# Kernel tuning notes

Hardware: AMD Instinct MI355X
Metric: run time of the kernel (lower is better)

The kernel has to match this reference:

```python
import jax, jax.numpy as jnp
import numpy as np

N_NODES = 100000
N_EDGES = 1600000
N_GRAPHS = 256
F_IN = 38
HID = 64


def graph_conv(x, edge_index, w_rel, b_rel, w_root):
    # PyG GraphConv (aggr='add'): out = lin_rel(sum_{j in N(i)} x_j) + lin_root(x_i)
    src, dst = edge_index[0], edge_index[1]
    agg = jax.ops.segment_sum(x[src], dst, num_segments=N_NODES)  # [N, F]
    return agg @ w_rel + b_rel + x @ w_root


def setup_inputs() -> dict:
    key = jax.random.key(0)
    ks = jax.random.split(key, 10)
    x = jax.random.normal(ks[0], (N_NODES, F_IN), dtype=jnp.float32)
    edge_index = jax.random.randint(ks[1], (2, N_EDGES), 0, N_NODES, dtype=jnp.int64)
    batch = jnp.sort(jax.random.randint(ks[2], (N_NODES,), 0, N_GRAPHS, dtype=jnp.int64))
    s1 = 1.0 / np.sqrt(F_IN)
    s2 = 1.0 / np.sqrt(HID)
    w1_rel = jax.random.uniform(ks[3], (F_IN, HID), jnp.float32, -s1, s1)
    b1_rel = jax.random.uniform(ks[4], (HID,), jnp.float32, -s1, s1)
    w1_root = jax.random.uniform(ks[5], (F_IN, HID), jnp.float32, -s1, s1)
    w2_rel = jax.random.uniform(ks[6], (HID, HID), jnp.float32, -s2, s2)
    b2_rel = jax.random.uniform(ks[7], (HID,), jnp.float32, -s2, s2)
    w2_root = jax.random.uniform(ks[8], (HID, HID), jnp.float32, -s2, s2)
    return {"x": x, "edge_index": edge_index, "batch": batch,
            "w1_rel": w1_rel, "b1_rel": b1_rel, "w1_root": w1_root,
            "w2_rel": w2_rel, "b2_rel": b2_rel, "w2_root": w2_root}


def reference(x, edge_index, batch, w1_rel, b1_rel, w1_root, w2_rel, b2_rel, w2_root):
    h = graph_conv(x, edge_index, w1_rel, b1_rel, w1_root)
    h = jax.nn.relu(h)
    h = graph_conv(h, edge_index, w2_rel, b2_rel, w2_root)
    # global_mean_pool: segment mean over batch ids
    sums = jax.ops.segment_sum(h, batch, num_segments=N_GRAPHS)  # [G, HID]
    counts = jax.ops.segment_sum(jnp.ones((N_NODES,), h.dtype), batch, num_segments=N_GRAPHS)
    pooled = sums / jnp.maximum(counts, 1.0)[:, None]
    # dropout(p=0.5, training=False) is identity in eval mode
    return jax.nn.relu(pooled)
```

## Files before the change

### kernel.cpp

```cpp
#include <hip/hip_runtime.h>

#define N_NODES 100000
#define N_EDGES 1600000
#define N_GRAPHS 256
#define F_IN 38
#define F_PAD 40
#define HID 64
#define CAPD 48

#define NB   391
#define EPB  4096
#define EDGE_BLOCKS 391
#define PACK_BLOCKS 1024
#define PACK_CHUNKS ((N_NODES + 1) * F_PAD / 8)
#define BCAP 4608
#define NBL  (2 * NB)

typedef unsigned short ushort;
typedef unsigned int uint;
typedef _Float16 h2 __attribute__((ext_vector_type(2)));

__device__ __forceinline__ h2 u2h(uint u) {
    union { uint u; h2 h; } v; v.u = u; return v.h;
}
__device__ __forceinline__ uint h2u(h2 h) {
    union { uint u; h2 h; } v; v.h = h; return v.u;
}
__device__ __forceinline__ ushort f2h_bits(float f) {
    union { _Float16 h; ushort s; } v; v.h = (_Float16)f; return v.s;
}
__device__ __forceinline__ int clampi(int v) {
    return (int)min((uint)v, (uint)N_NODES);
}

__global__ __launch_bounds__(256, 4) void pre_kernel(
        const float* __restrict__ x,
        const int* __restrict__ src,
        const int* __restrict__ dst,
        int* __restrict__ gcur,
        uint* __restrict__ ebuf,
        ushort* __restrict__ xb,
        ushort* __restrict__ hb) {
    __shared__ int    hist[NB];
    __shared__ int    offs[NB];
    __shared__ int    cur[NB];
    __shared__ int    gbase[NB];
    __shared__ int    scan[512];
    __shared__ uint   sbuf[EPB];
    __shared__ ushort sb[EPB];

    const int blk = blockIdx.x;
    if (blk >= EDGE_BLOCKS) {
        int gid = (blk - EDGE_BLOCKS) * 256 + threadIdx.x;
        if (gid < HID) hb[(N_NODES << 6) + gid] = 0;
        const int stride = PACK_BLOCKS * 256;
        for (int c = gid; c < PACK_CHUNKS; c += stride) {
            int n = c / 5;
            int f0 = (c - n * 5) * 8;
            ushort u[8];
            #pragma unroll
            for (int j = 0; j < 8; ++j) {
                int f = f0 + j;
                float v = (n < N_NODES && f < F_IN) ? x[n * F_IN + f] : 0.0f;
                u[j] = f2h_bits(v);
            }
            uint4 pk;
            pk.x = (uint)u[0] | ((uint)u[1] << 16);
            pk.y = (uint)u[2] | ((uint)u[3] << 16);
            pk.z = (uint)u[4] | ((uint)u[5] << 16);
            pk.w = (uint)u[6] | ((uint)u[7] << 16);
            *(uint4*)(xb + c * 8) = pk;
        }
        return;
    }

    for (int i = threadIdx.x; i < NB; i += 256) hist[i] = 0;
    __syncthreads();

    const int base = blk * EPB + threadIdx.x;
    int  bkt[EPB / 256];
    uint pl[EPB / 256];
    #pragma unroll
    for (int i = 0; i < EPB / 256; ++i) {
        int e = base + i * 256;
        bkt[i] = -1;
        if (e < N_EDGES) {
            int d = dst[e];
            bkt[i] = d >> 8;
            pl[i] = ((uint)src[e] << 8) | ((uint)d & 255u);
            atomicAdd(&hist[bkt[i]], 1);
        }
    }
    __syncthreads();

    {
        int i0 = threadIdx.x, i1 = threadIdx.x + 256;
        scan[i0] = (i0 < NB) ? hist[i0] : 0;
        scan[i1] = (i1 < NB) ? hist[i1] : 0;
        __syncthreads();
        for (int d = 1; d < 512; d <<= 1) {
            int v0 = (i0 >= d) ? scan[i0 - d] : 0;
            int v1 = (i1 >= d) ? scan[i1 - d] : 0;
            __syncthreads();
            scan[i0] += v0;
            scan[i1] += v1;
            __syncthreads();
        }
    }
    for (int i = threadIdx.x; i < NB; i += 256) {
        int h = hist[i];
        int o = scan[i] - h;
        offs[i] = o;
        cur[i] = o;
        gbase[i] = (h > 0) ? atomicAdd(&gcur[i], h) : 0;
    }
    __syncthreads();

    #pragma unroll
    for (int i = 0; i < EPB / 256; ++i) {
        if (bkt[i] >= 0) {
            int pos = atomicAdd(&cur[bkt[i]], 1);
            sbuf[pos] = pl[i];
            sb[pos] = (ushort)bkt[i];
        }
    }
    __syncthreads();

    int total = scan[NB - 1];
    for (int i = threadIdx.x; i < total; i += 256) {
        int b = sb[i];
        int p = gbase[b] + (i - offs[b]);
        if (p < BCAP) ebuf[b * BCAP + p] = sbuf[i];
    }
}

__global__ __launch_bounds__(512, 8) void layer1_kernel(
        const uint* __restrict__ xb32,
        const uint* __restrict__ ebuf,
        const int* __restrict__ gcur,
        const float* __restrict__ w_rel,
        const float* __restrict__ b_rel,
        const float* __restrict__ w_root,
        const int* __restrict__ batch,
        ushort* __restrict__ hb,
        float* __restrict__ hsum) {
    __shared__ uint s_wrelp[20 * HID];
    __shared__ uint s_wrootp[20 * HID];
    __shared__ int  s_slots[128 * CAPD];
    __shared__ int  cl[128];

    for (int i = threadIdx.x; i < 20 * HID; i += 512) {
        int kk = i >> 6, cc = i & 63;
        int k0 = 2 * kk, k1 = 2 * kk + 1;
        float r0 = (k0 < F_IN) ? w_rel[k0 * HID + cc] : 0.f;
        float r1 = (k1 < F_IN) ? w_rel[k1 * HID + cc] : 0.f;
        float o0 = (k0 < F_IN) ? w_root[k0 * HID + cc] : 0.f;
        float o1 = (k1 < F_IN) ? w_root[k1 * HID + cc] : 0.f;
        s_wrelp[i]  = (uint)f2h_bits(r0) | ((uint)f2h_bits(r1) << 16);
        s_wrootp[i] = (uint)f2h_bits(o0) | ((uint)f2h_bits(o1) << 16);
    }
    const int b   = blockIdx.x >> 1;
    const int dlo = (blockIdx.x & 1) << 7;
    if (threadIdx.x < 128) cl[threadIdx.x] = 0;
    {
        int4* sp = (int4*)s_slots;
        int4 dummy = make_int4(N_NODES, N_NODES, N_NODES, N_NODES);
        for (int i = threadIdx.x; i < 128 * CAPD / 4; i += 512) sp[i] = dummy;
    }
    __syncthreads();
    int e1 = gcur[b]; if (e1 > BCAP) e1 = BCAP;
    for (int idx = threadIdx.x; idx < e1; idx += 512) {
        uint e = ebuf[b * BCAP + idx];
        int dl = (int)(e & 255u) - dlo;
        if ((uint)dl < 128u) {
            int pos = atomicAdd(&cl[dl], 1);
            if (pos < CAPD) s_slots[dl * CAPD + pos] = (int)(e >> 8);
        }
    }
    __syncthreads();

    const int wave = threadIdx.x >> 6, lane = threadIdx.x & 63;
    const int half = lane >> 5, l32 = lane & 31;
    const int nbase = (b << 8) + dlo;

    h2   sums[8];
    uint xvs[8];
    #pragma unroll
    for (int i = 0; i < 8; ++i) {
        int nl = wave * 16 + 2 * i + half;
        int n = nbase + nl;
        uint xv = 0;
        int dp = 0;
        if (n < N_NODES) {
            int deg = cl[nl]; if (deg > CAPD) deg = CAPD;
            dp = (deg + 15) & ~15; if (dp > CAPD) dp = CAPD;
            if (l32 < 20) xv = xb32[n * 20 + l32];
        }
        h2 sum = {(_Float16)0, (_Float16)0};
        const int* sl = s_slots + nl * CAPD;
        for (int j = 0; j < dp; j += 16) {
            int4 a4 = *(const int4*)(sl + j);
            int4 b4 = *(const int4*)(sl + j + 4);
            int4 c4 = *(const int4*)(sl + j + 8);
            int4 d4 = *(const int4*)(sl + j + 12);
            if (l32 < 20) {
                uint v0 = xb32[clampi(a4.x) * 20 + l32];
                uint v1 = xb32[clampi(a4.y) * 20 + l32];
                uint v2 = xb32[clampi(a4.z) * 20 + l32];
                uint v3 = xb32[clampi(a4.w) * 20 + l32];
                uint v4 = xb32[clampi(b4.x) * 20 + l32];
                uint v5 = xb32[clampi(b4.y) * 20 + l32];
                uint v6 = xb32[clampi(b4.z) * 20 + l32];
                uint v7 = xb32[clampi(b4.w) * 20 + l32];
                uint v8 = xb32[clampi(c4.x) * 20 + l32];
                uint v9 = xb32[clampi(c4.y) * 20 + l32];
                uint va = xb32[clampi(c4.z) * 20 + l32];
                uint vb = xb32[clampi(c4.w) * 20 + l32];
                uint vc = xb32[clampi(d4.x) * 20 + l32];
                uint vd = xb32[clampi(d4.y) * 20 + l32];
                uint ve = xb32[clampi(d4.z) * 20 + l32];
                uint vf = xb32[clampi(d4.w) * 20 + l32];
                h2 t0 = (u2h(v0) + u2h(v1)) + (u2h(v2) + u2h(v3));
                h2 t1 = (u2h(v4) + u2h(v5)) + (u2h(v6) + u2h(v7));
                h2 t2 = (u2h(v8) + u2h(v9)) + (u2h(va) + u2h(vb));
                h2 t3 = (u2h(vc) + u2h(vd)) + (u2h(ve) + u2h(vf));
                sum += (t0 + t1) + (t2 + t3);
            }
        }
        sums[i] = sum;
        xvs[i] = xv;
    }
    __syncthreads();
    uint* s_a = (uint*)s_slots;
    uint* s_x = ((uint*)s_slots) + 128 * 20;
    #pragma unroll
    for (int i = 0; i < 8; ++i) {
        int nl = wave * 16 + 2 * i + half;
        if (l32 < 20) {
            s_a[nl * 20 + l32] = h2u(sums[i]);
            s_x[nl * 20 + l32] = xvs[i];
        }
    }
    __syncthreads();

    const int c = lane, r = wave;
    const float bias = b_rel[c];
    float psum = 0.f;
    int cur_g = -1;
    for (int i = 0; i < 16; ++i) {
        int nl = r * 16 + i;
        int n = nbase + nl;
        if (n >= N_NODES) break;
        h2 acc = {(_Float16)0, (_Float16)0};
        #pragma unroll
        for (int k8 = 0; k8 < 5; ++k8) {
            uint4 pa = *(const uint4*)&s_a[nl * 20 + k8 * 4];
            uint4 px = *(const uint4*)&s_x[nl * 20 + k8 * 4];
            acc += u2h(pa.x) * u2h(s_wrelp[(k8 * 4 + 0) * HID + c]);
            acc += u2h(pa.y) * u2h(s_wrelp[(k8 * 4 + 1) * HID + c]);
            acc += u2h(pa.z) * u2h(s_wrelp[(k8 * 4 + 2) * HID + c]);
            acc += u2h(pa.w) * u2h(s_wrelp[(k8 * 4 + 3) * HID + c]);
            acc += u2h(px.x) * u2h(s_wrootp[(k8 * 4 + 0) * HID + c]);
            acc += u2h(px.y) * u2h(s_wrootp[(k8 * 4 + 1) * HID + c]);
            acc += u2h(px.z) * u2h(s_wrootp[(k8 * 4 + 2) * HID + c]);
            acc += u2h(px.w) * u2h(s_wrootp[(k8 * 4 + 3) * HID + c]);
        }
        float hv = fmaxf((float)acc.x + (float)acc.y + bias, 0.f);
        hb[(n << 6) + c] = f2h_bits(hv);
        int g = batch[n];
        if (g != cur_g) {
            if (cur_g >= 0) atomicAdd(&hsum[(cur_g << 6) + c], psum);
            psum = 0.f;
            cur_g = g;
        }
        psum += hv;
    }
    if (cur_g >= 0) atomicAdd(&hsum[(cur_g << 6) + c], psum);
}

__global__ __launch_bounds__(256, 8) void layer2_kernel(
        const uint* __restrict__ hb32,
        const uint* __restrict__ ebuf,
        const int* __restrict__ gcur,
        const int* __restrict__ batch,
        float* __restrict__ esum) {
    __shared__ int   s_batch[256];
    __shared__ float s_acc[4 * 64];

    const int b = blockIdx.x >> 2;
    const int q = blockIdx.x & 3;
    const int nbase = b << 8;
    {
        int n = nbase + threadIdx.x;
        s_batch[threadIdx.x] = (n < N_NODES) ? batch[n] : (N_GRAPHS - 1);
    }
    s_acc[threadIdx.x] = 0.f;
    __syncthreads();
    const int g0 = s_batch[0];

    int e1 = gcur[b]; if (e1 > BCAP) e1 = BCAP;
    const int lo = (e1 * q) >> 2;
    const int hi = (e1 * (q + 1)) >> 2;

    const int wave = threadIdx.x >> 6, lane = threadIdx.x & 63;
    const int hf = lane >> 5, l32 = lane & 31;
    const uint* eb = ebuf + b * BCAP;

    float a0x = 0.f, a0y = 0.f, a1x = 0.f, a1y = 0.f;
    float a2x = 0.f, a2y = 0.f, a3x = 0.f, a3y = 0.f;

    for (int base = lo + (wave << 6); base < hi; base += 256) {
        int cnt = hi - base; if (cnt > 64) cnt = 64;
        uint pv = (lane < cnt) ? eb[base + lane] : 0u;
        #pragma unroll 8
        for (int k = 0; k < 32; ++k) {
            int idx2 = 2 * k + hf;
            uint p = __shfl(pv, idx2, 64);
            if (idx2 < cnt) {
                int srcn = (int)(p >> 8);
                int g = s_batch[p & 255u];
                int off = g - g0;
                h2 hv = u2h(hb32[(srcn << 5) + l32]);
                float hx = (float)hv.x, hy = (float)hv.y;
                if (off == 0)      { a0x += hx; a0y += hy; }
                else if (off == 1) { a1x += hx; a1y += hy; }
                else if (off == 2) { a2x += hx; a2y += hy; }
                else if (off == 3) { a3x += hx; a3y += hy; }
                else {
                    atomicAdd(&esum[(g << 6) + 2 * l32], hx);
                    atomicAdd(&esum[(g << 6) + 2 * l32 + 1], hy);
                }
            }
        }
    }
    atomicAdd(&s_acc[0 * 64 + 2 * l32],     a0x);
    atomicAdd(&s_acc[0 * 64 + 2 * l32 + 1], a0y);
    atomicAdd(&s_acc[1 * 64 + 2 * l32],     a1x);
    atomicAdd(&s_acc[1 * 64 + 2 * l32 + 1], a1y);
    atomicAdd(&s_acc[2 * 64 + 2 * l32],     a2x);
    atomicAdd(&s_acc[2 * 64 + 2 * l32 + 1], a2y);
    atomicAdd(&s_acc[3 * 64 + 2 * l32],     a3x);
    atomicAdd(&s_acc[3 * 64 + 2 * l32 + 1], a3y);
    __syncthreads();
    {
        int off = threadIdx.x >> 6, ch = threadIdx.x & 63;
        int g = g0 + off;
        float v = s_acc[off * 64 + ch];
        if (v != 0.f && g < N_GRAPHS)
            atomicAdd(&esum[(g << 6) + ch], v);
    }
}

__global__ void finalize_kernel(const float* __restrict__ esum,
                                const float* __restrict__ hsum,
                                const float* __restrict__ w2_rel,
                                const float* __restrict__ w2_root,
                                const float* __restrict__ b2,
                                const int* __restrict__ batch,
                                float* __restrict__ out) {
    __shared__ float s_e[HID];
    __shared__ float s_h[HID];
    const int g = blockIdx.x;
    const int c = threadIdx.x;
    s_e[c] = esum[(g << 6) + c];
    s_h[c] = hsum[(g << 6) + c];
    __syncthreads();

    int lo = 0, hi = N_NODES;
    while (lo < hi) { int m = (lo + hi) >> 1; if (batch[m] < g) lo = m + 1; else hi = m; }
    int start = lo;
    hi = N_NODES;
    while (lo < hi) { int m = (lo + hi) >> 1; if (batch[m] < g + 1) lo = m + 1; else hi = m; }
    int cntg = lo - start;

    float acc = (float)cntg * b2[c];
    #pragma unroll
    for (int k = 0; k < HID; ++k) {
        acc += s_e[k] * w2_rel[k * HID + c];
        acc += s_h[k] * w2_root[k * HID + c];
    }
    float denom = cntg > 0 ? (float)cntg : 1.f;
    out[(g << 6) + c] = fmaxf(acc / denom, 0.f);
}

extern "C" void kernel_launch(void* const* d_in, const int* in_sizes, int n_in,
                              void* d_out, int out_size, void* d_ws, size_t ws_size,
                              hipStream_t stream) {
    const float* x       = (const float*)d_in[0];
    const int*   ei      = (const int*)  d_in[1];
    const int*   batch   = (const int*)  d_in[2];
    const float* w1_rel  = (const float*)d_in[3];
    const float* b1_rel  = (const float*)d_in[4];
    const float* w1_root = (const float*)d_in[5];
    const float* w2_rel  = (const float*)d_in[6];
    const float* b2_rel  = (const float*)d_in[7];
    const float* w2_root = (const float*)d_in[8];
    float* out = (float*)d_out;

    const int* src = ei;
    const int* dst = ei + N_EDGES;

    char* wsb = (char*)d_ws;
    float*  hsum  = (float*) (wsb);
    float*  esum  = (float*) (wsb + 65536);
    int*    gcur  = (int*)   (wsb + 131072);
    uint*   ebuf  = (uint*)  (wsb + 132672);
    ushort* xb    = (ushort*)(wsb + 19732640);
    ushort* hb    = (ushort*)(wsb + 27732720);

    hipMemsetAsync(wsb, 0, 132636, stream);

    {
        pre_kernel<<<EDGE_BLOCKS + PACK_BLOCKS, 256, 0, stream>>>(
            x, src, dst, gcur, ebuf, xb, hb);
    }
    {
        layer1_kernel<<<NBL, 512, 0, stream>>>((const uint*)xb, ebuf, gcur,
                                               w1_rel, b1_rel, w1_root, batch,
                                               hb, hsum);
    }
    {
        layer2_kernel<<<4 * NB, 256, 0, stream>>>((const uint*)hb, ebuf, gcur,
                                                  batch, esum);
    }
    {
        finalize_kernel<<<N_GRAPHS, HID, 0, stream>>>(esum, hsum, w2_rel, w2_root,
                                                      b2_rel, batch, out);
    }
}
```

Baseline: 253.7 us.

## Partition layer2 edge gathers by source-node range for cache locality

Layer2 blocks now split each destination bucket's edges by source-node range (8 partitions) instead of by contiguous edge quarters. Each block scans all edges in its bucket, compacts the ones whose source falls in its partition into shared memory via ballot, then gathers from that subset. The goal is to keep concurrently running blocks' gathers within a smaller region of hb so they hit in L2/MALL. The cost is that every edge list is read 8 times, and there are extra syncs and twice as many blocks.

```diff
diff --git a/kernel.cpp b/kernel.cpp
--- a/kernel.cpp
+++ b/kernel.cpp
@@ -15,6 +15,9 @@
 #define PACK_CHUNKS ((N_NODES + 1) * F_PAD / 8)
 #define BCAP 4608
 #define NBL  (2 * NB)
+
+#define NPART 8
+#define PDIV  12500
 
 typedef unsigned short ushort;
 typedef unsigned int uint;
@@ -285,10 +288,12 @@
         const int* __restrict__ batch,
         float* __restrict__ esum) {
     __shared__ int   s_batch[256];
+    __shared__ uint  s_sel[2048];
     __shared__ float s_acc[4 * 64];
-
-    const int b = blockIdx.x >> 2;
-    const int q = blockIdx.x & 3;
+    __shared__ int   s_cnt;
+
+    const int b = blockIdx.x >> 3;
+    const int p = blockIdx.x & 7;
     const int nbase = b << 8;
     {
         int n = nbase + threadIdx.x;
@@ -297,42 +302,66 @@
     s_acc[threadIdx.x] = 0.f;
     __syncthreads();
     const int g0 = s_batch[0];
-
+    const uint slo = (uint)(p * PDIV);
+    const uint shi = slo + PDIV;
+
+    const uint* eb = ebuf + b * BCAP;
     int e1 = gcur[b]; if (e1 > BCAP) e1 = BCAP;
-    const int lo = (e1 * q) >> 2;
-    const int hi = (e1 * (q + 1)) >> 2;
 
     const int wave = threadIdx.x >> 6, lane = threadIdx.x & 63;
-    const int hf = lane >> 5, l32 = lane & 31;
-    const uint* eb = ebuf + b * BCAP;
+    const int hw = threadIdx.x >> 5;
+    const int l32 = threadIdx.x & 31;
 
     float a0x = 0.f, a0y = 0.f, a1x = 0.f, a1y = 0.f;
     float a2x = 0.f, a2y = 0.f, a3x = 0.f, a3y = 0.f;
 
-    for (int base = lo + (wave << 6); base < hi; base += 256) {
-        int cnt = hi - base; if (cnt > 64) cnt = 64;
-        uint pv = (lane < cnt) ? eb[base + lane] : 0u;
-        #pragma unroll 8
-        for (int k = 0; k < 32; ++k) {
-            int idx2 = 2 * k + hf;
-            uint p = __shfl(pv, idx2, 64);
-            if (idx2 < cnt) {
-                int srcn = (int)(p >> 8);
-                int g = s_batch[p & 255u];
-                int off = g - g0;
-                h2 hv = u2h(hb32[(srcn << 5) + l32]);
-                float hx = (float)hv.x, hy = (float)hv.y;
-                if (off == 0)      { a0x += hx; a0y += hy; }
-                else if (off == 1) { a1x += hx; a1y += hy; }
-                else if (off == 2) { a2x += hx; a2y += hy; }
-                else if (off == 3) { a3x += hx; a3y += hy; }
-                else {
-                    atomicAdd(&esum[(g << 6) + 2 * l32], hx);
-                    atomicAdd(&esum[(g << 6) + 2 * l32 + 1], hy);
+    for (int cbase = 0; cbase < e1; cbase += 2048) {
+        if (threadIdx.x == 0) s_cnt = 0;
+        __syncthreads();
+        const int chi = min(cbase + 2048, e1);
+        for (int off = cbase + (wave << 6); off < chi; off += 256) {
+            int e = off + lane;
+            uint pl = 0;
+            bool ok = false;
+            if (e < chi) {
+                pl = eb[e];
+                uint s = pl >> 8;
+                ok = (s >= slo) && (s < shi);
+            }
+            unsigned long long mask = __ballot(ok);
+            int nsel = (int)__popcll(mask);
+            if (nsel) {
+                int bs = 0;
+                if (lane == 0) bs = atomicAdd(&s_cnt, nsel);
+                bs = __shfl(bs, 0, 64);
+                if (ok) {
+                    int pos = bs + (int)__popcll(mask & ((1ull << lane) - 1ull));
+                    s_sel[pos] = pl;
                 }
             }
         }
-    }
+        __syncthreads();
+        const int scnt = s_cnt;
+        #pragma unroll 8
+        for (int i = hw; i < scnt; i += 8) {
+            uint pl = s_sel[i];
+            int srcn = (int)(pl >> 8);
+            int g = s_batch[pl & 255u];
+            int off = g - g0;
+            h2 hv = u2h(hb32[(srcn << 5) + l32]);
+            float hx = (float)hv.x, hy = (float)hv.y;
+            if (off == 0)      { a0x += hx; a0y += hy; }
+            else if (off == 1) { a1x += hx; a1y += hy; }
+            else if (off == 2) { a2x += hx; a2y += hy; }
+            else if (off == 3) { a3x += hx; a3y += hy; }
+            else {
+                atomicAdd(&esum[(g << 6) + 2 * l32], hx);
+                atomicAdd(&esum[(g << 6) + 2 * l32 + 1], hy);
+            }
+        }
+        __syncthreads();
+    }
+
     atomicAdd(&s_acc[0 * 64 + 2 * l32],     a0x);
     atomicAdd(&s_acc[0 * 64 + 2 * l32 + 1], a0y);
     atomicAdd(&s_acc[1 * 64 + 2 * l32],     a1x);
@@ -420,7 +449,7 @@
                                                hb, hsum);
     }
     {
-        layer2_kernel<<<4 * NB, 256, 0, stream>>>((const uint*)hb, ebuf, gcur,
+        layer2_kernel<<<8 * NB, 256, 0, stream>>>((const uint*)hb, ebuf, gcur,
                                                   batch, esum);
     }
     {
```

Measured after the change: 265.8 us. 1.05x slower.
